# Performance work log

Hardware: AMD Instinct MI355X
Metric: run time of the kernel (lower is better)

## Reference

```python
import jax, jax.numpy as jnp
import numpy as np

NUM_HEADS = 16
D_MODEL = 1024
B, T = 2, 2048


def setup_inputs() -> dict:
    key = jax.random.key(0)
    ks = jax.random.split(key, 5)
    s = 1.0 / np.sqrt(D_MODEL)
    return {
        "x": jax.random.normal(ks[0], (B, T, D_MODEL), dtype=jnp.float32),
        "Wq": jax.random.normal(ks[1], (D_MODEL, D_MODEL), dtype=jnp.float32) * s,
        "Wk": jax.random.normal(ks[2], (D_MODEL, D_MODEL), dtype=jnp.float32) * s,
        "Wv": jax.random.normal(ks[3], (D_MODEL, D_MODEL), dtype=jnp.float32) * s,
        "Wo": jax.random.normal(ks[4], (D_MODEL, D_MODEL), dtype=jnp.float32) * s,
    }


def reference(x, Wq, Wk, Wv, Wo):
    # x: [B, T, D]; W*: [D, D] (torch nn.Linear weight layout, y = x @ W.T)
    b, t, d = x.shape
    h = NUM_HEADS
    hd = d // h

    def split_heads(y):
        # [B, T, D] -> [B, H, T, hd]
        return y.reshape(b, t, h, hd).transpose(0, 2, 1, 3)

    q = split_heads(x @ Wq.T)
    k = split_heads(x @ Wk.T)
    v = split_heads(x @ Wv.T)

    # scale uses last dim AFTER head split: 1/sqrt(head_dim)
    scores = jnp.einsum("bhqd,bhkd->bhqk", q, k) / jnp.sqrt(jnp.asarray(hd, x.dtype))
    causal = jnp.tril(jnp.ones((t, t), dtype=bool))  # [T, T]
    scores = jnp.where(causal[None, None], scores, -jnp.inf)
    attn = jax.nn.softmax(scores, axis=-1)  # [B, H, T, T]

    out = jnp.einsum("bhqk,bhkd->bhqd", attn, v)  # [B, H, T, hd]
    out = out.transpose(0, 2, 1, 3).reshape(b, t, d)  # concat heads
    return out @ Wo.T
```

## Files before the change

### kernel.cpp

```cpp
#include <hip/hip_runtime.h>
#include <hip/hip_bf16.h>

#define T_SEQ 2048
#define DM    1024
#define MTOT  4096

typedef short v8s __attribute__((ext_vector_type(8)));
typedef short v4s __attribute__((ext_vector_type(4)));
typedef float v4f __attribute__((ext_vector_type(4)));

__device__ __forceinline__ unsigned short f2bf(float f) {
  union { float f; unsigned int u; } x; x.f = f;
  return (unsigned short)((x.u + (((x.u >> 16) & 1u) + 0x7fffu)) >> 16);
}

__device__ __forceinline__ unsigned int pk2(float a, float b) {
  unsigned int ua = __float_as_uint(a) + 0x8000u;
  unsigned int ub = __float_as_uint(b) + 0x8000u;
  return __builtin_amdgcn_perm(ub, ua, 0x07060302u);
}

__device__ __forceinline__ v8s pack8bf(v4f a, v4f b) {
  union { v8s s; unsigned int u[4]; } o;
  o.u[0] = pk2(a[0], a[1]);
  o.u[1] = pk2(a[2], a[3]);
  o.u[2] = pk2(b[0], b[1]);
  o.u[3] = pk2(b[2], b[3]);
  return o.s;
}

__device__ __forceinline__ float fast_exp2(float x) {
#if __has_builtin(__builtin_amdgcn_exp2f)
  return __builtin_amdgcn_exp2f(x);
#else
  return exp2f(x);
#endif
}

__device__ __forceinline__ void gload16(const void* g, void* lds) {
  __builtin_amdgcn_global_load_lds(
      (const __attribute__((address_space(1))) unsigned int*)g,
      (__attribute__((address_space(3))) unsigned int*)lds, 16, 0, 0);
}

__global__ __launch_bounds__(256) void convert_all(
    const float* __restrict__ x,
    const float* __restrict__ Wq, const float* __restrict__ Wk,
    const float* __restrict__ Wv, const float* __restrict__ Wo,
    unsigned short* __restrict__ xb, unsigned short* __restrict__ wb)
{
  int i = blockIdx.x * 256 + threadIdx.x;
  const float4* src;
  ushort4* dst;
  int idx;
  if (i < (1 << 20)) {
    src = (const float4*)x; dst = (ushort4*)xb; idx = i;
  } else {
    int j = i - (1 << 20);
    int wsel = j >> 18;
    idx = j & ((1 << 18) - 1);
    const float* s = (wsel == 0) ? Wq : (wsel == 1) ? Wk : (wsel == 2) ? Wv : Wo;
    src = (const float4*)s;
    dst = (ushort4*)(wb + (size_t)wsel * DM * DM);
  }
  float4 v = src[idx];
  ushort4 o = { f2bf(v.x), f2bf(v.y), f2bf(v.z), f2bf(v.w) };
  dst[idx] = o;
}

__global__ __launch_bounds__(256) void qkv_fused2(
    const unsigned short* __restrict__ xb,
    const unsigned short* __restrict__ wb,
    unsigned short* __restrict__ Qw, unsigned short* __restrict__ Kw,
    unsigned short* __restrict__ Vtw)
{
  __shared__ unsigned short smem[20480];
  unsigned short* As = smem;

  const int tid  = threadIdx.x;
  const int wv   = tid >> 6, l = tid & 63;
  const int lrow = l & 15, lq = l >> 4;
  const int wm = wv >> 1;
  const int wn = wv & 1;
  const int srow = l >> 3, sslot = l & 7;
  const int swz  = sslot ^ (srow & 7);
  const int m0 = blockIdx.x * 128, n0 = blockIdx.y * 64;

  v4f acc[3][4][2];
#pragma unroll
  for (int z = 0; z < 3; ++z)
#pragma unroll
    for (int mt = 0; mt < 4; ++mt)
#pragma unroll
      for (int nt = 0; nt < 2; ++nt) acc[z][mt][nt] = (v4f){0.f, 0.f, 0.f, 0.f};

  const size_t aBase = (size_t)(m0 + wv * 32 + srow) * DM + swz * 8;
  const size_t bBase = (size_t)(n0 + wv * 16 + srow) * DM + swz * 8;

  for (int k0 = 0; k0 < DM; k0 += 64) {
    __syncthreads();
#pragma unroll
    for (int i = 0; i < 4; ++i)
      gload16(xb + aBase + (size_t)i * 8 * DM + k0, As + (wv * 32 + i * 8) * 64);
#pragma unroll
    for (int z = 0; z < 3; ++z)
#pragma unroll
      for (int i = 0; i < 2; ++i)
        gload16(wb + (size_t)z * DM * DM + bBase + (size_t)i * 8 * DM + k0,
                smem + 8192 + z * 4096 + (wv * 16 + i * 8) * 64);
    __syncthreads();
#pragma unroll
    for (int kc = 0; kc < 2; ++kc) {
      const int aslot = ((kc << 2) | lq) ^ (lrow & 7);
      v8s af[4];
#pragma unroll
      for (int mt = 0; mt < 4; ++mt)
        af[mt] = *(const v8s*)&As[(wm * 64 + mt * 16 + lrow) * 64 + aslot * 8];
#pragma unroll
      for (int z = 0; z < 3; ++z) {
        const unsigned short* Bz = smem + 8192 + z * 4096;
        v8s bf[2];
#pragma unroll
        for (int nt = 0; nt < 2; ++nt)
          bf[nt] = *(const v8s*)&Bz[(wn * 32 + nt * 16 + lrow) * 64 + aslot * 8];
#pragma unroll
        for (int mt = 0; mt < 4; ++mt)
#pragma unroll
          for (int nt = 0; nt < 2; ++nt)
            acc[z][mt][nt] = __builtin_amdgcn_mfma_f32_16x16x32_bf16(
                af[mt], bf[nt], acc[z][mt][nt], 0, 0, 0);
      }
    }
  }

#pragma unroll
  for (int z = 0; z < 2; ++z) {
    unsigned short* Y = z ? Kw : Qw;
#pragma unroll
    for (int mt = 0; mt < 4; ++mt)
#pragma unroll
      for (int nt = 0; nt < 2; ++nt)
#pragma unroll
        for (int r = 0; r < 4; ++r) {
          int row = m0 + wm * 64 + mt * 16 + lq * 4 + r;
          int col = n0 + wn * 32 + nt * 16 + lrow;
          Y[(size_t)row * DM + col] = f2bf(acc[z][mt][nt][r]);
        }
  }

  __syncthreads();
#pragma unroll
  for (int mt = 0; mt < 4; ++mt)
#pragma unroll
    for (int nt = 0; nt < 2; ++nt)
#pragma unroll
      for (int r = 0; r < 4; ++r) {
        int trow = wm * 64 + mt * 16 + lq * 4 + r;
        int col  = wn * 32 + nt * 16 + lrow;
        int slot = (col >> 3) ^ (trow & 7);
        smem[trow * 64 + slot * 8 + (col & 7)] = f2bf(acc[2][mt][nt][r]);
      }
  __syncthreads();
  {
    const int d = tid & 63;
    const int quarter = tid >> 6;
    const int bb = m0 >> 11;
    const int tblk = (m0 & 2047) >> 7;
    const int h = n0 >> 6;
    const int bh = bb * 16 + h;
    unsigned short* dst = Vtw + (((size_t)bh * 16 + tblk) * 64 + d) * 128;
    const int ch = d >> 3, e7 = d & 7;
#pragma unroll
    for (int jj = 0; jj < 4; ++jj) {
      unsigned short vals[8];
#pragma unroll
      for (int e = 0; e < 8; ++e) {
        int st = quarter * 32 + (e >> 2) * 16 + jj * 4 + (e & 3);
        vals[e] = smem[st * 64 + (ch ^ (st & 7)) * 8 + e7];
      }
      *(v8s*)(dst + (quarter * 4 + jj) * 8) = *(const v8s*)vals;
    }
  }
}

__global__ __launch_bounds__(256) void oproj_gemm2(
    const unsigned short* __restrict__ AO,
    const unsigned short* __restrict__ Wob,
    float* __restrict__ Y)
{
  __shared__ unsigned short smem[12288];
  unsigned short* As = smem;
  unsigned short* Bs = smem + 4096;

  const int tid  = threadIdx.x;
  const int wv   = tid >> 6, l = tid & 63;
  const int lrow = l & 15, lq = l >> 4;
  const int wm = wv >> 1;
  const int wn = wv & 1;
  const int srow = l >> 3, sslot = l & 7;
  const int swz  = sslot ^ (srow & 7);
  const int m0 = blockIdx.x * 64, n0 = blockIdx.y * 128;

  v4f acc[2][4];
#pragma unroll
  for (int mt = 0; mt < 2; ++mt)
#pragma unroll
    for (int nt = 0; nt < 4; ++nt) acc[mt][nt] = (v4f){0.f, 0.f, 0.f, 0.f};

  const size_t aBase = (size_t)(m0 + wv * 16 + srow) * DM + swz * 8;
  const size_t bBase = (size_t)(n0 + wv * 32 + srow) * DM + swz * 8;

  for (int k0 = 0; k0 < DM; k0 += 64) {
    __syncthreads();
#pragma unroll
    for (int i = 0; i < 2; ++i)
      gload16(AO + aBase + (size_t)i * 8 * DM + k0, As + (wv * 16 + i * 8) * 64);
#pragma unroll
    for (int i = 0; i < 4; ++i)
      gload16(Wob + bBase + (size_t)i * 8 * DM + k0, Bs + (wv * 32 + i * 8) * 64);
    __syncthreads();
#pragma unroll
    for (int kc = 0; kc < 2; ++kc) {
      const int aslot = ((kc << 2) | lq) ^ (lrow & 7);
      v8s af[2], bf[4];
#pragma unroll
      for (int mt = 0; mt < 2; ++mt)
        af[mt] = *(const v8s*)&As[(wm * 32 + mt * 16 + lrow) * 64 + aslot * 8];
#pragma unroll
      for (int nt = 0; nt < 4; ++nt)
        bf[nt] = *(const v8s*)&Bs[(wn * 64 + nt * 16 + lrow) * 64 + aslot * 8];
#pragma unroll
      for (int mt = 0; mt < 2; ++mt)
#pragma unroll
        for (int nt = 0; nt < 4; ++nt)
          acc[mt][nt] = __builtin_amdgcn_mfma_f32_16x16x32_bf16(
              af[mt], bf[nt], acc[mt][nt], 0, 0, 0);
    }
  }
#pragma unroll
  for (int mt = 0; mt < 2; ++mt)
#pragma unroll
    for (int nt = 0; nt < 4; ++nt)
#pragma unroll
      for (int r = 0; r < 4; ++r) {
        int row = m0 + wm * 32 + mt * 16 + lq * 4 + r;
        int col = n0 + wn * 64 + nt * 16 + lrow;
        Y[(size_t)row * DM + col] = acc[mt][nt][r];
      }
}

__global__ __launch_bounds__(256) void attn7(
    const unsigned short* __restrict__ Q,
    const unsigned short* __restrict__ K,
    const unsigned short* __restrict__ Vt,
    unsigned short* __restrict__ O)
{
  __shared__ unsigned short Ks[256 * 64];
  __shared__ unsigned short VtsA[64 * 128];
  __shared__ unsigned short VtsB[64 * 128];

  const int tid  = threadIdx.x;
  const int wave = tid >> 6;
  const int lane = tid & 63;
  const int lrow = lane & 15;
  const int lq   = lane >> 4;
  const int gid  = blockIdx.x;
  const int qt   = 31 - (gid >> 5);
  const int bh   = gid & 31;
  const int b = bh >> 4, h = bh & 15;

  union { v8s s; unsigned int u[4]; } ones;
  ones.u[0] = 0x3F803F80u; ones.u[1] = 0x3F803F80u;
  ones.u[2] = 0x3F803F80u; ones.u[3] = 0x3F803F80u;

  const int qrow = qt * 64 + wave * 16 + lrow;
  const unsigned short* qp = Q + ((size_t)(b * T_SEQ + qrow)) * DM + h * 64;
  v8s qf0 = *(const v8s*)(qp + lq * 8);
  v8s qf1 = *(const v8s*)(qp + 32 + lq * 8);

  v4f oacc[4];
#pragma unroll
  for (int dt = 0; dt < 4; ++dt) oacc[dt] = (v4f){0.f, 0.f, 0.f, 0.f};
  v4f sacc = {0.f, 0.f, 0.f, 0.f};

  const int nkt = (qt >> 2) + 1;
  const int qmax = qt * 64 + 63;

  const int kchunk = (lane & 7) ^ ((lane >> 3) & 7);
  const unsigned short* kg =
      K + ((size_t)(b * T_SEQ) + wave * 8 + (lane >> 3)) * DM + h * 64 + kchunk * 8;
  unsigned short* kdst = Ks + (wave * 8) * 64;
  const int vd = wave * 4 + (lane >> 4);
  const int vslot = lane & 15;
  const int vchunk = (vslot & 8) | ((vslot & 7) ^ (vd & 7));
  const unsigned short* vg =
      Vt + ((size_t)bh * 1024 + vd) * 128 + vchunk * 8;
  unsigned short* vdstA = VtsA + (wave * 4) * 128;
  unsigned short* vdstB = VtsB + (wave * 4) * 128;

  const int slot0 = lq ^ (lrow & 7);
  const int slot1 = (4 + lq) ^ (lrow & 7);

  for (int kt = 0; kt < nkt; ++kt) {
    __syncthreads();
#pragma unroll
    for (int i = 0; i < 8; ++i)
      gload16(kg + ((size_t)kt * 256 + i * 32) * DM, kdst + i * 32 * 64);
#pragma unroll
    for (int i = 0; i < 4; ++i)
      gload16(vg + (size_t)kt * 16384 + i * 2048, vdstA + i * 16 * 128);
#pragma unroll
    for (int i = 0; i < 4; ++i)
      gload16(vg + (size_t)kt * 16384 + 8192 + i * 2048, vdstB + i * 16 * 128);
    __syncthreads();

#pragma unroll
    for (int sub = 0; sub < 2; ++sub) {
      const int kb = kt * 256 + sub * 128;
      if (kb > qmax) break;
      const unsigned short* Kss = Ks + sub * 128 * 64;
      const unsigned short* Vts = sub ? VtsB : VtsA;

      v4f s[8];
#pragma unroll
      for (int nt = 0; nt < 8; ++nt) {
        v4f a = {0.f, 0.f, 0.f, 0.f};
        v8s k0 = *(const v8s*)&Kss[(nt * 16 + lrow) * 64 + slot0 * 8];
        a = __builtin_amdgcn_mfma_f32_16x16x32_bf16(k0, qf0, a, 0, 0, 0);
        v8s k1 = *(const v8s*)&Kss[(nt * 16 + lrow) * 64 + slot1 * 8];
        a = __builtin_amdgcn_mfma_f32_16x16x32_bf16(k1, qf1, a, 0, 0, 0);
        s[nt] = a;
      }

      const bool needmask = (kb + 127 > qt * 64 + wave * 16);
      if (needmask) {
#pragma unroll
        for (int nt = 0; nt < 8; ++nt)
#pragma unroll
          for (int r = 0; r < 4; ++r) {
            float p = fast_exp2(fmaf(s[nt][r], 0.18033688f, -23.0831206f));
            if (kb + nt * 16 + lq * 4 + r > qt * 64 + wave * 16 + lrow) p = 0.f;
            s[nt][r] = p;
          }
      } else {
#pragma unroll
        for (int nt = 0; nt < 8; ++nt)
#pragma unroll
          for (int r = 0; r < 4; ++r)
            s[nt][r] = fast_exp2(fmaf(s[nt][r], 0.18033688f, -23.0831206f));
      }

      v8s pf[4];
#pragma unroll
      for (int kp = 0; kp < 4; ++kp) pf[kp] = pack8bf(s[2 * kp], s[2 * kp + 1]);

#pragma unroll
      for (int kp = 0; kp < 4; ++kp) {
        sacc = __builtin_amdgcn_mfma_f32_16x16x32_bf16(ones.s, pf[kp], sacc, 0, 0, 0);
#pragma unroll
        for (int dt = 0; dt < 4; ++dt) {
          int ch = kp * 4 + lq;
          int slot = (ch & 8) | ((ch & 7) ^ (lrow & 7));
          v8s vv = *(const v8s*)&Vts[(dt * 16 + lrow) * 128 + slot * 8];
          oacc[dt] = __builtin_amdgcn_mfma_f32_16x16x32_bf16(
              vv, pf[kp], oacc[dt], 0, 0, 0);
        }
      }
    }
  }

  const float rinv = 1.0f / sacc[0];

  const int token = qt * 64 + wave * 16 + lrow;
  unsigned short* op = O + ((size_t)(b * T_SEQ + token)) * DM + h * 64;
#pragma unroll
  for (int dt = 0; dt < 4; ++dt) {
    union { v4s s; unsigned int u[2]; } o;
    o.u[0] = pk2(oacc[dt][0] * rinv, oacc[dt][1] * rinv);
    o.u[1] = pk2(oacc[dt][2] * rinv, oacc[dt][3] * rinv);
    *(v4s*)(op + dt * 16 + lq * 4) = o.s;
  }
}

extern "C" void kernel_launch(void* const* d_in, const int* in_sizes, int n_in,
                              void* d_out, int out_size, void* d_ws, size_t ws_size,
                              hipStream_t stream) {
  const float* x  = (const float*)d_in[0];
  const float* Wq = (const float*)d_in[1];
  const float* Wk = (const float*)d_in[2];
  const float* Wv = (const float*)d_in[3];
  const float* Wo = (const float*)d_in[4];
  float* out = (float*)d_out;

  unsigned short* xb  = (unsigned short*)d_ws;
  unsigned short* wb  = xb + (size_t)MTOT * DM;
  unsigned short* Qw  = wb + (size_t)4 * DM * DM;
  unsigned short* Kw  = Qw + (size_t)MTOT * DM;
  unsigned short* Vtw = Kw + (size_t)MTOT * DM;
  unsigned short* AO  = xb;

  convert_all<<<8192, 256, 0, stream>>>(x, Wq, Wk, Wv, Wo, xb, wb);
  qkv_fused2<<<dim3(32, 16), 256, 0, stream>>>(xb, wb, Qw, Kw, Vtw);
  attn7<<<1024, 256, 0, stream>>>(Qw, Kw, Vtw, AO);
  oproj_gemm2<<<dim3(64, 8), 256, 0, stream>>>(AO, wb + (size_t)3 * DM * DM, out);
}
```

Measured before the change: 162.0 us.

## Double-buffer K/V tiles in attention and raise wave priority around MFMA blocks

The attention kernel moves from a single 256-key LDS stage, loaded and then synchronised before compute, to 128-key tiles in two ping-pong LDS buffers. The next tile's async global-to-LDS load is issued before computing the current one, which overlaps memory latency with MFMA work and drops one barrier per tile. It also wraps the QK and PV MFMA sections in s_setprio to favour matrix-issuing waves. LDS use stays the same, but each block now runs more, smaller iterations. The prefetch is written into the other buffer with no explicit wait on its completion before the barrier, so correctness depends on how gload16 waits.

Result: no change. 163.2 us (+0.7%).

```diff
diff --git a/kernel.cpp b/kernel.cpp
--- a/kernel.cpp
+++ b/kernel.cpp
@@ -249,15 +249,14 @@
       }
 }
 
-__global__ __launch_bounds__(256) void attn7(
+__global__ __launch_bounds__(256) void attn8(
     const unsigned short* __restrict__ Q,
     const unsigned short* __restrict__ K,
     const unsigned short* __restrict__ Vt,
     unsigned short* __restrict__ O)
 {
-  __shared__ unsigned short Ks[256 * 64];
-  __shared__ unsigned short VtsA[64 * 128];
-  __shared__ unsigned short VtsB[64 * 128];
+  __shared__ unsigned short Ks[2][128 * 64];
+  __shared__ unsigned short Vts[2][64 * 128];
 
   const int tid  = threadIdx.x;
   const int wave = tid >> 6;
@@ -283,91 +282,98 @@
   for (int dt = 0; dt < 4; ++dt) oacc[dt] = (v4f){0.f, 0.f, 0.f, 0.f};
   v4f sacc = {0.f, 0.f, 0.f, 0.f};
 
-  const int nkt = (qt >> 2) + 1;
-  const int qmax = qt * 64 + 63;
+  const int n128 = (qt >> 1) + 1;
 
   const int kchunk = (lane & 7) ^ ((lane >> 3) & 7);
   const unsigned short* kg =
       K + ((size_t)(b * T_SEQ) + wave * 8 + (lane >> 3)) * DM + h * 64 + kchunk * 8;
-  unsigned short* kdst = Ks + (wave * 8) * 64;
   const int vd = wave * 4 + (lane >> 4);
   const int vslot = lane & 15;
   const int vchunk = (vslot & 8) | ((vslot & 7) ^ (vd & 7));
   const unsigned short* vg =
       Vt + ((size_t)bh * 1024 + vd) * 128 + vchunk * 8;
-  unsigned short* vdstA = VtsA + (wave * 4) * 128;
-  unsigned short* vdstB = VtsB + (wave * 4) * 128;
 
   const int slot0 = lq ^ (lrow & 7);
   const int slot1 = (4 + lq) ^ (lrow & 7);
 
-  for (int kt = 0; kt < nkt; ++kt) {
-    __syncthreads();
-#pragma unroll
-    for (int i = 0; i < 8; ++i)
-      gload16(kg + ((size_t)kt * 256 + i * 32) * DM, kdst + i * 32 * 64);
-#pragma unroll
-    for (int i = 0; i < 4; ++i)
-      gload16(vg + (size_t)kt * 16384 + i * 2048, vdstA + i * 16 * 128);
-#pragma unroll
-    for (int i = 0; i < 4; ++i)
-      gload16(vg + (size_t)kt * 16384 + 8192 + i * 2048, vdstB + i * 16 * 128);
-    __syncthreads();
-
-#pragma unroll
-    for (int sub = 0; sub < 2; ++sub) {
-      const int kb = kt * 256 + sub * 128;
-      if (kb > qmax) break;
-      const unsigned short* Kss = Ks + sub * 128 * 64;
-      const unsigned short* Vts = sub ? VtsB : VtsA;
-
-      v4f s[8];
-#pragma unroll
-      for (int nt = 0; nt < 8; ++nt) {
-        v4f a = {0.f, 0.f, 0.f, 0.f};
-        v8s k0 = *(const v8s*)&Kss[(nt * 16 + lrow) * 64 + slot0 * 8];
-        a = __builtin_amdgcn_mfma_f32_16x16x32_bf16(k0, qf0, a, 0, 0, 0);
-        v8s k1 = *(const v8s*)&Kss[(nt * 16 + lrow) * 64 + slot1 * 8];
-        a = __builtin_amdgcn_mfma_f32_16x16x32_bf16(k1, qf1, a, 0, 0, 0);
-        s[nt] = a;
+#define STAGE(tt, buf) do {                                                   \
+    unsigned short* kd_ = Ks[buf] + (wave * 8) * 64;                          \
+    _Pragma("unroll")                                                         \
+    for (int i_ = 0; i_ < 4; ++i_)                                            \
+      gload16(kg + ((size_t)(tt) * 128 + i_ * 32) * DM, kd_ + i_ * 32 * 64);  \
+    unsigned short* vd_ = Vts[buf] + (wave * 4) * 128;                        \
+    _Pragma("unroll")                                                         \
+    for (int i_ = 0; i_ < 4; ++i_)                                            \
+      gload16(vg + (size_t)(tt) * 8192 + i_ * 2048, vd_ + i_ * 16 * 128);     \
+  } while (0)
+
+  STAGE(0, 0);
+  __syncthreads();
+
+  int cur = 0;
+  for (int tt = 0; tt < n128; ++tt) {
+    if (tt + 1 < n128) STAGE(tt + 1, cur ^ 1);
+
+    const int kb = tt * 128;
+    const unsigned short* Kss = Ks[cur];
+    const unsigned short* Vss = Vts[cur];
+
+    v4f s[8];
+    __builtin_amdgcn_s_setprio(1);
+#pragma unroll
+    for (int nt = 0; nt < 8; ++nt) {
+      v4f a = {0.f, 0.f, 0.f, 0.f};
+      v8s k0 = *(const v8s*)&Kss[(nt * 16 + lrow) * 64 + slot0 * 8];
+      a = __builtin_amdgcn_mfma_f32_16x16x32_bf16(k0, qf0, a, 0, 0, 0);
+      v8s k1 = *(const v8s*)&Kss[(nt * 16 + lrow) * 64 + slot1 * 8];
+      a = __builtin_amdgcn_mfma_f32_16x16x32_bf16(k1, qf1, a, 0, 0, 0);
+      s[nt] = a;
+    }
+    __builtin_amdgcn_s_setprio(0);
+
+    const bool needmask = (kb + 127 > qt * 64 + wave * 16);
+    if (needmask) {
+#pragma unroll
+      for (int nt = 0; nt < 8; ++nt)
+#pragma unroll
+        for (int r = 0; r < 4; ++r) {
+          float p = fast_exp2(fmaf(s[nt][r], 0.18033688f, -23.0831206f));
+          if (kb + nt * 16 + lq * 4 + r > qt * 64 + wave * 16 + lrow) p = 0.f;
+          s[nt][r] = p;
+        }
+    } else {
+#pragma unroll
+      for (int nt = 0; nt < 8; ++nt)
+#pragma unroll
+        for (int r = 0; r < 4; ++r)
+          s[nt][r] = fast_exp2(fmaf(s[nt][r], 0.18033688f, -23.0831206f));
+    }
+
+    v8s pf[4];
+#pragma unroll
+    for (int kp = 0; kp < 4; ++kp) pf[kp] = pack8bf(s[2 * kp], s[2 * kp + 1]);
+
+    __builtin_amdgcn_s_setprio(1);
+#pragma unroll
+    for (int kp = 0; kp < 4; ++kp) {
+      sacc = __builtin_amdgcn_mfma_f32_16x16x32_bf16(ones.s, pf[kp], sacc, 0, 0, 0);
+#pragma unroll
+      for (int dt = 0; dt < 4; ++dt) {
+        int ch = kp * 4 + lq;
+        int slot = (ch & 8) | ((ch & 7) ^ (lrow & 7));
+        v8s vv = *(const v8s*)&Vss[(dt * 16 + lrow) * 128 + slot * 8];
+        oacc[dt] = __builtin_amdgcn_mfma_f32_16x16x32_bf16(
+            vv, pf[kp], oacc[dt], 0, 0, 0);
       }
-
-      const bool needmask = (kb + 127 > qt * 64 + wave * 16);
-      if (needmask) {
-#pragma unroll
-        for (int nt = 0; nt < 8; ++nt)
-#pragma unroll
-          for (int r = 0; r < 4; ++r) {
-            float p = fast_exp2(fmaf(s[nt][r], 0.18033688f, -23.0831206f));
-            if (kb + nt * 16 + lq * 4 + r > qt * 64 + wave * 16 + lrow) p = 0.f;
-            s[nt][r] = p;
-          }
-      } else {
-#pragma unroll
-        for (int nt = 0; nt < 8; ++nt)
-#pragma unroll
-          for (int r = 0; r < 4; ++r)
-            s[nt][r] = fast_exp2(fmaf(s[nt][r], 0.18033688f, -23.0831206f));
-      }
-
-      v8s pf[4];
-#pragma unroll
-      for (int kp = 0; kp < 4; ++kp) pf[kp] = pack8bf(s[2 * kp], s[2 * kp + 1]);
-
-#pragma unroll
-      for (int kp = 0; kp < 4; ++kp) {
-        sacc = __builtin_amdgcn_mfma_f32_16x16x32_bf16(ones.s, pf[kp], sacc, 0, 0, 0);
-#pragma unroll
-        for (int dt = 0; dt < 4; ++dt) {
-          int ch = kp * 4 + lq;
-          int slot = (ch & 8) | ((ch & 7) ^ (lrow & 7));
-          v8s vv = *(const v8s*)&Vts[(dt * 16 + lrow) * 128 + slot * 8];
-          oacc[dt] = __builtin_amdgcn_mfma_f32_16x16x32_bf16(
-              vv, pf[kp], oacc[dt], 0, 0, 0);
-        }
-      }
-    }
-  }
+    }
+    __builtin_amdgcn_s_setprio(0);
+
+    if (tt + 1 < n128) {
+      __syncthreads();
+      cur ^= 1;
+    }
+  }
+#undef STAGE
 
   const float rinv = 1.0f / sacc[0];
 
@@ -401,6 +407,6 @@
 
   convert_all<<<8192, 256, 0, stream>>>(x, Wq, Wk, Wv, Wo, xb, wb);
   qkv_fused2<<<dim3(32, 16), 256, 0, stream>>>(xb, wb, Qw, Kw, Vtw);
-  attn7<<<1024, 256, 0, stream>>>(Qw, Kw, Vtw, AO);
+  attn8<<<1024, 256, 0, stream>>>(Qw, Kw, Vtw, AO);
   oproj_gemm2<<<dim3(64, 8), 256, 0, stream>>>(AO, wb + (size_t)3 * DM * DM, out);
 }
```
